# Kernel optimization log

Hardware: AMD Instinct MI355X
Metric: run time of the kernel (lower is better)

The kernel has to match this reference:

```python
import jax, jax.numpy as jnp
import numpy as np

HIDDEN = 4096
NUM_HEADS = 32
NUM_KV_HEADS = 8
HEAD_DIM = 128


def setup_inputs() -> dict:
    key = jax.random.key(0)
    k0, k1, k2, k3, k4 = jax.random.split(key, 5)
    B, S = 1, 2048
    s = 0.02
    return {
        "hidden_states": jax.random.normal(k0, (B, S, HIDDEN), dtype=jnp.float32),
        "Wq": jax.random.normal(k1, (HIDDEN, NUM_HEADS * HEAD_DIM), dtype=jnp.float32) * s,
        "Wk": jax.random.normal(k2, (HIDDEN, NUM_KV_HEADS * HEAD_DIM), dtype=jnp.float32) * s,
        "Wv": jax.random.normal(k3, (HIDDEN, NUM_KV_HEADS * HEAD_DIM), dtype=jnp.float32) * s,
        "Wo": jax.random.normal(k4, (NUM_HEADS * HEAD_DIM, HIDDEN), dtype=jnp.float32) * s,
    }


def reference(hidden_states, Wq, Wk, Wv, Wo):
    B, S, _ = hidden_states.shape
    n_rep = NUM_HEADS // NUM_KV_HEADS
    # Projections -> [B, H, S, D]
    q = (hidden_states @ Wq).reshape(B, S, NUM_HEADS, HEAD_DIM).transpose(0, 2, 1, 3)
    k = (hidden_states @ Wk).reshape(B, S, NUM_KV_HEADS, HEAD_DIM).transpose(0, 2, 1, 3)
    v = (hidden_states @ Wv).reshape(B, S, NUM_KV_HEADS, HEAD_DIM).transpose(0, 2, 1, 3)
    # GQA expansion: repeat_interleave KV heads to match query head count
    k = jnp.repeat(k, n_rep, axis=1)
    v = jnp.repeat(v, n_rep, axis=1)
    scale = HEAD_DIM ** -0.5
    # Full [B, H, S, S] attention scores (faithful to the naive reference)
    scores = jnp.einsum("bhqd,bhkd->bhqk", q, k) * scale
    causal = jnp.tril(jnp.ones((S, S), dtype=bool))
    scores = jnp.where(causal[None, None], scores, jnp.float32(-jnp.inf))
    probs = jax.nn.softmax(scores, axis=-1)
    out = jnp.einsum("bhqk,bhkd->bhqd", probs, v)
    out = out.transpose(0, 2, 1, 3).reshape(B, S, NUM_HEADS * HEAD_DIM)
    return out @ Wo
```

## Files before the change

kernel.cpp:

```cpp
#include <hip/hip_runtime.h>
#include <hip/hip_bf16.h>

typedef __bf16 bf16;
typedef __bf16 bf16x4 __attribute__((ext_vector_type(4)));
typedef __bf16 bf16x8 __attribute__((ext_vector_type(8)));
typedef float  f32x4  __attribute__((ext_vector_type(4)));
typedef float  f32x16 __attribute__((ext_vector_type(16)));
typedef unsigned u32x4 __attribute__((ext_vector_type(4)));

#define SEQ  2048
#define HID  4096
#define QKVN 6144

__device__ __forceinline__ void gload_lds16(const void* g, void* l) {
  __builtin_amdgcn_global_load_lds(
      (const __attribute__((address_space(1))) void*)g,
      (__attribute__((address_space(3))) void*)l, 16, 0, 0);
}

__device__ __forceinline__ unsigned cvtpk(float lo, float hi) {
  unsigned r;
  asm("v_cvt_pk_bf16_f32 %0, %1, %2" : "=v"(r) : "v"(lo), "v"(hi));
  return r;
}
__device__ __forceinline__ void plswap(unsigned& a, unsigned& b) {
  asm("v_permlane32_swap_b32 %0, %1" : "+v"(a), "+v"(b));
}

__global__ __launch_bounds__(256) void cast_f32_bf16(const float* __restrict__ in,
                                                     bf16* __restrict__ out, int n) {
  int i = (blockIdx.x * 256 + threadIdx.x) * 4;
  int stride = gridDim.x * 256 * 4;
  for (; i < n; i += stride) {
    float4 v = *(const float4*)(in + i);
    bf16x4 o;
    o[0] = (bf16)v.x; o[1] = (bf16)v.y; o[2] = (bf16)v.z; o[3] = (bf16)v.w;
    *(bf16x4*)(out + i) = o;
  }
}

__global__ __launch_bounds__(256) void transpose_cast(const float* __restrict__ W,
                                                      bf16* __restrict__ Wt,
                                                      int N, int roff) {
  __shared__ float tile[64][65];
  int k0 = blockIdx.y * 64;
  int n0 = blockIdx.x * 64;
  int t = threadIdx.x;
  int lr = t >> 4;
  int lc = (t & 15) * 4;
#pragma unroll
  for (int p = 0; p < 4; ++p) {
    int row = p * 16 + lr;
    float4 v = *(const float4*)(W + (size_t)(k0 + row) * N + n0 + lc);
    tile[row][lc] = v.x; tile[row][lc + 1] = v.y;
    tile[row][lc + 2] = v.z; tile[row][lc + 3] = v.w;
  }
  __syncthreads();
#pragma unroll
  for (int p = 0; p < 4; ++p) {
    int n = p * 16 + lr;
    bf16x4 o;
#pragma unroll
    for (int q = 0; q < 4; ++q) o[q] = (bf16)tile[lc + q][n];
    *(bf16x4*)(Wt + (size_t)(roff + n0 + n) * 4096 + k0 + lc) = o;
  }
}

__global__ __launch_bounds__(256) void transpose_v(const bf16* __restrict__ QKV,
                                                   bf16* __restrict__ Vt_g) {
  __shared__ bf16 tile[32][33];
  int s0 = blockIdx.x * 32;
  int d0 = blockIdx.y * 32;
  int g  = blockIdx.z;
  int t = threadIdx.x;
  int r = t >> 5, c = t & 31;
#pragma unroll
  for (int p = 0; p < 4; ++p)
    tile[r + p * 8][c] = QKV[(size_t)(s0 + r + p * 8) * QKVN + 5120 + g * 128 + d0 + c];
  __syncthreads();
#pragma unroll
  for (int p = 0; p < 4; ++p)
    Vt_g[(size_t)(g * 128 + d0 + r + p * 8) * SEQ + s0 + c] = tile[c][r + p * 8];
}

template <typename OUT_T>
__global__ __launch_bounds__(256) void gemm_bt(const bf16* __restrict__ A,
                                               const bf16* __restrict__ Bt,
                                               OUT_T* __restrict__ C,
                                               int K, int ldc) {
  __shared__ __align__(16) bf16 Abuf[128 * 64];
  __shared__ __align__(16) bf16 Bbuf[128 * 64];
  int m0 = blockIdx.y * 128, n0 = blockIdx.x * 128;
  int tid = threadIdx.x, w = tid >> 6, lane = tid & 63;
  int wr = w >> 1, wc = w & 1;
  int l15 = lane & 15, l4 = lane >> 4;
  f32x4 acc[4][4] = {};
  const int nk = K >> 6;
  for (int kt = 0; kt < nk; ++kt) {
    int k0 = kt << 6;
#pragma unroll
    for (int p = 0; p < 4; ++p) {
      int c = p * 256 + tid;
      int row = c >> 3, slot = c & 7;
      int ssl = (slot ^ (row & 7)) << 4;
      gload_lds16((const char*)(A + (size_t)(m0 + row) * K + k0) + ssl, (char*)Abuf + c * 16);
      gload_lds16((const char*)(Bt + (size_t)(n0 + row) * K + k0) + ssl, (char*)Bbuf + c * 16);
    }
    __syncthreads();
    bf16x8 af[4][2], bfr[4][2];
#pragma unroll
    for (int m = 0; m < 4; ++m)
#pragma unroll
      for (int kk = 0; kk < 2; ++kk) {
        int row = wr * 64 + m * 16 + l15;
        af[m][kk] = *(const bf16x8*)((const char*)Abuf + row * 128 +
                                     (((kk * 4 + l4) ^ (row & 7)) << 4));
      }
#pragma unroll
    for (int n = 0; n < 4; ++n)
#pragma unroll
      for (int kk = 0; kk < 2; ++kk) {
        int row = wc * 64 + n * 16 + l15;
        bfr[n][kk] = *(const bf16x8*)((const char*)Bbuf + row * 128 +
                                      (((kk * 4 + l4) ^ (row & 7)) << 4));
      }
#pragma unroll
    for (int kk = 0; kk < 2; ++kk)
#pragma unroll
      for (int m = 0; m < 4; ++m)
#pragma unroll
        for (int n = 0; n < 4; ++n)
          acc[m][n] = __builtin_amdgcn_mfma_f32_16x16x32_bf16(af[m][kk], bfr[n][kk],
                                                              acc[m][n], 0, 0, 0);
    __syncthreads();
  }
#pragma unroll
  for (int m = 0; m < 4; ++m)
#pragma unroll
    for (int n = 0; n < 4; ++n)
#pragma unroll
      for (int i = 0; i < 4; ++i) {
        int row = m0 + wr * 64 + m * 16 + l4 * 4 + i;
        int col = n0 + wc * 64 + n * 16 + l15;
        C[(size_t)row * ldc + col] = (OUT_T)acc[m][n][i];
      }
}

__global__ __launch_bounds__(256, 2) void attn_kernel(const bf16* __restrict__ QKV,
                                                      const bf16* __restrict__ Vt_g,
                                                      bf16* __restrict__ attn) {
  __shared__ __align__(16) bf16 Klds[2][64 * 128];
  __shared__ __align__(16) bf16 Vlds[2][64 * 128];
  const int bid = blockIdx.x;
  const int g = bid & 7;
  const int rest = bid >> 3;
  const int hi = rest & 3;
  const int pair = rest >> 2;
  const int qb_a = pair, qb_b = 31 - pair;
  const int tid = threadIdx.x, w = tid >> 6, lane = tid & 63;
  const int l31 = lane & 31, hh = lane >> 5;
  const int head = g * 4 + hi;
  const bool isB = (w < 2);
  const int myqb = isB ? qb_b : qb_a;
  const int unit_q0 = myqb * 64 + (w & 1) * 32;
  const int qcol = head * 128;
  const int kcol = 4096 + g * 128;
  const float scale = 0.08838834764831845f;
  const float LOG2E = 1.4426950408889634f;

  const bf16* Vhead = Vt_g + (size_t)g * 128 * SEQ;

  bf16x8 qf[8];
#pragma unroll
  for (int db = 0; db < 8; ++db)
    qf[db] = *(const bf16x8*)(QKV + (size_t)(unit_q0 + l31) * QKVN + qcol +
                              db * 16 + hh * 8);

  f32x16 acc_o[4] = {};
  float m_run = -1e30f, l_run = 0.f;

  auto stageKV = [&](int kb, int buf) {
#pragma unroll
    for (int j = 0; j < 4; ++j) {
      int c = tid + (j << 8);
      int row = c >> 4, s = c & 15;
      int sl = s ^ (row & 15);
      gload_lds16((const char*)(QKV + (size_t)(kb + row) * QKVN + kcol) + (sl << 4),
                  (char*)Klds[buf] + (c << 4));
      int d = row * 2 + (sl >> 3);
      int ko = (sl & 7) << 3;
      gload_lds16(Vhead + (size_t)d * SEQ + kb + ko, (char*)Vlds[buf] + (c << 4));
    }
  };

  auto compute_unit = [&](int kb, int cur) {
    const char* Kb = (const char*)Klds[cur];
    const char* Vb = (const char*)Vlds[cur];
    f32x16 s0 = {}, s1 = {};
    __builtin_amdgcn_s_setprio(1);
#pragma unroll
    for (int db = 0; db < 8; ++db) {
      int slot = (db * 2 + hh) ^ (l31 & 15);
      bf16x8 k0 = *(const bf16x8*)(Kb + l31 * 256 + slot * 16);
      bf16x8 k1 = *(const bf16x8*)(Kb + (32 + l31) * 256 + slot * 16);
      s0 = __builtin_amdgcn_mfma_f32_32x32x16_bf16(k0, qf[db], s0, 0, 0, 0);
      s1 = __builtin_amdgcn_mfma_f32_32x32x16_bf16(k1, qf[db], s1, 0, 0, 0);
    }
    __builtin_amdgcn_s_setprio(0);
    float p0[16], p1[16];
    const bool needmask = (kb + 64 > unit_q0);
    const int qg = unit_q0 + l31;
#pragma unroll
    for (int r = 0; r < 16; ++r) {
      float v0 = s0[r] * scale, v1 = s1[r] * scale;
      if (needmask) {
        int krow = (r & 3) + 8 * (r >> 2) + 4 * hh;
        if (kb + krow > qg)      v0 = -1e30f;
        if (kb + 32 + krow > qg) v1 = -1e30f;
      }
      p0[r] = v0; p1[r] = v1;
    }
    float t = fmaxf(p0[0], p1[0]);
#pragma unroll
    for (int r = 1; r < 16; ++r) t = fmaxf(t, fmaxf(p0[r], p1[r]));
    t = fmaxf(t, __shfl_xor(t, 32));
    if (!__all(t - m_run <= 8.0f)) {
      float mnew = fmaxf(m_run, t);
      float fac = exp2f((m_run - mnew) * LOG2E);
      m_run = mnew;
      l_run *= fac;
#pragma unroll
      for (int dt = 0; dt < 4; ++dt)
#pragma unroll
        for (int r = 0; r < 16; ++r) acc_o[dt][r] *= fac;
    }
    float psum = 0.f;
#pragma unroll
    for (int r = 0; r < 16; ++r) {
      p0[r] = exp2f((p0[r] - m_run) * LOG2E); psum += p0[r];
      p1[r] = exp2f((p1[r] - m_run) * LOG2E); psum += p1[r];
    }
    psum += __shfl_xor(psum, 32);
    l_run += psum;
    bf16x8 paf[4];
#pragma unroll
    for (int kstep = 0; kstep < 4; ++kstep) {
      const float* p = (kstep < 2) ? p0 : p1;
      const int base = (kstep & 1) * 8;
      unsigned a0 = cvtpk(p[base + 0], p[base + 1]);
      unsigned b0 = cvtpk(p[base + 4], p[base + 5]);
      plswap(a0, b0);
      unsigned a1 = cvtpk(p[base + 2], p[base + 3]);
      unsigned b1 = cvtpk(p[base + 6], p[base + 7]);
      plswap(a1, b1);
      u32x4 pw; pw[0] = a0; pw[1] = a1; pw[2] = b0; pw[3] = b1;
      paf[kstep] = __builtin_bit_cast(bf16x8, pw);
    }
    __builtin_amdgcn_s_setprio(1);
#pragma unroll
    for (int dt = 0; dt < 4; ++dt) {
      int vrow = dt * 16 + (l31 >> 1);
#pragma unroll
      for (int kstep = 0; kstep < 4; ++kstep) {
        int slot = ((l31 & 1) * 8 + kstep * 2 + hh) ^ (vrow & 15);
        bf16x8 vf = *(const bf16x8*)(Vb + vrow * 256 + slot * 16);
        acc_o[dt] = __builtin_amdgcn_mfma_f32_32x32x16_bf16(vf, paf[kstep], acc_o[dt], 0, 0, 0);
      }
    }
    __builtin_amdgcn_s_setprio(0);
  };

  stageKV(0, 0);
  __syncthreads();

  int cur = 0;
  for (int kbi = 0; kbi <= qb_b; ++kbi) {
    int kb = kbi * 64;
    if (kbi < qb_b) stageKV(kb + 64, cur ^ 1);
    if (isB || kbi <= qb_a) compute_unit(kb, cur);
    __syncthreads();
    cur ^= 1;
  }

  float inv_l = 1.0f / l_run;
  bf16* orow = attn + (size_t)(unit_q0 + l31) * 4096 + qcol;
#pragma unroll
  for (int dt = 0; dt < 4; ++dt)
#pragma unroll
    for (int r = 0; r < 16; ++r) {
      int d = dt * 32 + (r & 3) + 8 * (r >> 2) + 4 * hh;
      orow[d] = (bf16)(acc_o[dt][r] * inv_l);
    }
}

extern "C" void kernel_launch(void* const* d_in, const int* in_sizes, int n_in,
                              void* d_out, int out_size, void* d_ws, size_t ws_size,
                              hipStream_t stream) {
  const float* X  = (const float*)d_in[0];
  const float* Wq = (const float*)d_in[1];
  const float* Wk = (const float*)d_in[2];
  const float* Wv = (const float*)d_in[3];
  const float* Wo = (const float*)d_in[4];
  float* out = (float*)d_out;

  const size_t XB_OFF  = 0;
  const size_t WT_OFF  = 16777216;
  const size_t VT_OFF  = WT_OFF + 33554432;
  const size_t QKV_OFF = 16777216 + 50331648;
  if (ws_size < (size_t)92274688) return;

  char* ws = (char*)d_ws;
  bf16* Xb    = (bf16*)(ws + XB_OFF);
  bf16* Wt    = (bf16*)(ws + WT_OFF);
  bf16* Vt_g  = (bf16*)(ws + VT_OFF);
  bf16* QKV   = (bf16*)(ws + QKV_OFF);
  bf16* attnb = Xb;

  cast_f32_bf16<<<2048, 256, 0, stream>>>(X, Xb, SEQ * HID);
  transpose_cast<<<dim3(4096 / 64, 4096 / 64), 256, 0, stream>>>(Wq, Wt, 4096, 0);
  transpose_cast<<<dim3(1024 / 64, 4096 / 64), 256, 0, stream>>>(Wk, Wt, 1024, 4096);
  transpose_cast<<<dim3(1024 / 64, 4096 / 64), 256, 0, stream>>>(Wv, Wt, 1024, 5120);
  gemm_bt<bf16><<<dim3(QKVN / 128, SEQ / 128), 256, 0, stream>>>(Xb, Wt, QKV, HID, QKVN);
  transpose_cast<<<dim3(4096 / 64, 4096 / 64), 256, 0, stream>>>(Wo, Wt, 4096, 0);
  transpose_v<<<dim3(SEQ / 32, 4, 8), 256, 0, stream>>>(QKV, Vt_g);
  attn_kernel<<<512, 256, 0, stream>>>(QKV, Vt_g, attnb);
  gemm_bt<float><<<dim3(4096 / 128, SEQ / 128), 256, 0, stream>>>(attnb, Wt, out, HID, 4096);
}
```

Before: 369.8 us.

## Fuse weight transpose and bf16 cast into GEMM B-tile loads

Drops the separate transpose_cast kernels for Wq/Wk/Wv/Wo. The GEMMs now read the fp32 weights directly in their natural K-major layout, convert them to bf16 in registers, store them to LDS, and fetch MFMA B fragments with ds_read_b64_tr_b16 transposed LDS reads. This removes a full read/write pass over 64 MB of fp32 weights and the bf16 Wt workspace. In exchange each GEMM block reads fp32 weights (twice the bytes) on every tile, once per M-block, through synchronous register loads instead of async global_load_lds.

```diff
diff --git a/kernel.cpp b/kernel.cpp
--- a/kernel.cpp
+++ b/kernel.cpp
@@ -7,6 +7,7 @@
 typedef float  f32x4  __attribute__((ext_vector_type(4)));
 typedef float  f32x16 __attribute__((ext_vector_type(16)));
 typedef unsigned u32x4 __attribute__((ext_vector_type(4)));
+typedef __attribute__((address_space(3))) char lds_char;
 
 #define SEQ  2048
 #define HID  4096
@@ -39,33 +40,6 @@
   }
 }
 
-__global__ __launch_bounds__(256) void transpose_cast(const float* __restrict__ W,
-                                                      bf16* __restrict__ Wt,
-                                                      int N, int roff) {
-  __shared__ float tile[64][65];
-  int k0 = blockIdx.y * 64;
-  int n0 = blockIdx.x * 64;
-  int t = threadIdx.x;
-  int lr = t >> 4;
-  int lc = (t & 15) * 4;
-#pragma unroll
-  for (int p = 0; p < 4; ++p) {
-    int row = p * 16 + lr;
-    float4 v = *(const float4*)(W + (size_t)(k0 + row) * N + n0 + lc);
-    tile[row][lc] = v.x; tile[row][lc + 1] = v.y;
-    tile[row][lc + 2] = v.z; tile[row][lc + 3] = v.w;
-  }
-  __syncthreads();
-#pragma unroll
-  for (int p = 0; p < 4; ++p) {
-    int n = p * 16 + lr;
-    bf16x4 o;
-#pragma unroll
-    for (int q = 0; q < 4; ++q) o[q] = (bf16)tile[lc + q][n];
-    *(bf16x4*)(Wt + (size_t)(roff + n0 + n) * 4096 + k0 + lc) = o;
-  }
-}
-
 __global__ __launch_bounds__(256) void transpose_v(const bf16* __restrict__ QKV,
                                                    bf16* __restrict__ Vt_g) {
   __shared__ bf16 tile[32][33];
@@ -84,30 +58,57 @@
 }
 
 template <typename OUT_T>
-__global__ __launch_bounds__(256) void gemm_bt(const bf16* __restrict__ A,
-                                               const bf16* __restrict__ Bt,
-                                               OUT_T* __restrict__ C,
-                                               int K, int ldc) {
+__global__ __launch_bounds__(256) void gemm_trb(const bf16* __restrict__ A,
+                                                const float* __restrict__ W0,
+                                                const float* __restrict__ W1,
+                                                const float* __restrict__ W2,
+                                                OUT_T* __restrict__ C,
+                                                int K, int ldc) {
   __shared__ __align__(16) bf16 Abuf[128 * 64];
-  __shared__ __align__(16) bf16 Bbuf[128 * 64];
+  __shared__ __align__(16) bf16 Bbuf[64 * 128];
   int m0 = blockIdx.y * 128, n0 = blockIdx.x * 128;
+  const float* W; int Wn, n0l;
+  if (n0 < 4096)      { W = W0; Wn = 4096; n0l = n0; }
+  else if (n0 < 5120) { W = W1; Wn = 1024; n0l = n0 - 4096; }
+  else                { W = W2; Wn = 1024; n0l = n0 - 5120; }
   int tid = threadIdx.x, w = tid >> 6, lane = tid & 63;
   int wr = w >> 1, wc = w & 1;
   int l15 = lane & 15, l4 = lane >> 4;
   f32x4 acc[4][4] = {};
+  lds_char* const bbase = (lds_char*)(char*)Bbuf + wc * 512 + l4 * 2048 + l15 * 8;
   const int nk = K >> 6;
   for (int kt = 0; kt < nk; ++kt) {
     int k0 = kt << 6;
+    float4 bv0[4], bv1[4];
+#pragma unroll
+    for (int p = 0; p < 4; ++p) {
+      int c = p * 256 + tid;
+      int kq = c >> 4, n8 = (c & 15) * 8;
+      const float* src = W + (size_t)(k0 + kq) * Wn + n0l + n8;
+      bv0[p] = *(const float4*)src;
+      bv1[p] = *(const float4*)(src + 4);
+    }
 #pragma unroll
     for (int p = 0; p < 4; ++p) {
       int c = p * 256 + tid;
       int row = c >> 3, slot = c & 7;
       int ssl = (slot ^ (row & 7)) << 4;
       gload_lds16((const char*)(A + (size_t)(m0 + row) * K + k0) + ssl, (char*)Abuf + c * 16);
-      gload_lds16((const char*)(Bt + (size_t)(n0 + row) * K + k0) + ssl, (char*)Bbuf + c * 16);
+    }
+#pragma unroll
+    for (int p = 0; p < 4; ++p) {
+      int c = p * 256 + tid;
+      int kq = c >> 4, n8 = (c & 15) * 8;
+      u32x4 pw;
+      pw[0] = cvtpk(bv0[p].x, bv0[p].y);
+      pw[1] = cvtpk(bv0[p].z, bv0[p].w);
+      pw[2] = cvtpk(bv1[p].x, bv1[p].y);
+      pw[3] = cvtpk(bv1[p].z, bv1[p].w);
+      int boff = (kq >> 2) * 1024 + (n8 >> 4) * 128 + (kq & 3) * 32 + (n8 & 15) * 2;
+      *(u32x4*)((char*)Bbuf + boff) = pw;
     }
     __syncthreads();
-    bf16x8 af[4][2], bfr[4][2];
+    bf16x8 af[4][2];
 #pragma unroll
     for (int m = 0; m < 4; ++m)
 #pragma unroll
@@ -116,13 +117,29 @@
         af[m][kk] = *(const bf16x8*)((const char*)Abuf + row * 128 +
                                      (((kk * 4 + l4) ^ (row & 7)) << 4));
       }
-#pragma unroll
-    for (int n = 0; n < 4; ++n)
+    unsigned long long tr[4][2][2];
+#pragma unroll
+    for (int nf = 0; nf < 4; ++nf)
+#pragma unroll
+      for (int kk = 0; kk < 2; ++kk)
+#pragma unroll
+        for (int h = 0; h < 2; ++h)
+          asm volatile("ds_read_b64_tr_b16 %0, %1 offset:%c2"
+                       : "=v"(tr[nf][kk][h])
+                       : "v"(bbase), "i"(kk * 8192 + h * 1024 + nf * 128));
+    asm volatile("s_waitcnt lgkmcnt(0)" ::: "memory");
+    __builtin_amdgcn_sched_barrier(0);
+    bf16x8 bfr[4][2];
+#pragma unroll
+    for (int nf = 0; nf < 4; ++nf)
 #pragma unroll
       for (int kk = 0; kk < 2; ++kk) {
-        int row = wc * 64 + n * 16 + l15;
-        bfr[n][kk] = *(const bf16x8*)((const char*)Bbuf + row * 128 +
-                                      (((kk * 4 + l4) ^ (row & 7)) << 4));
+        u32x4 pw;
+        pw[0] = (unsigned)(tr[nf][kk][0]);
+        pw[1] = (unsigned)(tr[nf][kk][0] >> 32);
+        pw[2] = (unsigned)(tr[nf][kk][1]);
+        pw[3] = (unsigned)(tr[nf][kk][1] >> 32);
+        bfr[nf][kk] = __builtin_bit_cast(bf16x8, pw);
       }
 #pragma unroll
     for (int kk = 0; kk < 2; ++kk)
@@ -304,25 +321,21 @@
   float* out = (float*)d_out;
 
   const size_t XB_OFF  = 0;
-  const size_t WT_OFF  = 16777216;
-  const size_t VT_OFF  = WT_OFF + 33554432;
-  const size_t QKV_OFF = 16777216 + 50331648;
-  if (ws_size < (size_t)92274688) return;
+  const size_t VT_OFF  = 16777216;
+  const size_t QKV_OFF = 16777216 + 4194304;
+  if (ws_size < (size_t)(QKV_OFF + 25165824)) return;
 
   char* ws = (char*)d_ws;
   bf16* Xb    = (bf16*)(ws + XB_OFF);
-  bf16* Wt    = (bf16*)(ws + WT_OFF);
   bf16* Vt_g  = (bf16*)(ws + VT_OFF);
   bf16* QKV   = (bf16*)(ws + QKV_OFF);
   bf16* attnb = Xb;
 
   cast_f32_bf16<<<2048, 256, 0, stream>>>(X, Xb, SEQ * HID);
-  transpose_cast<<<dim3(4096 / 64, 4096 / 64), 256, 0, stream>>>(Wq, Wt, 4096, 0);
-  transpose_cast<<<dim3(1024 / 64, 4096 / 64), 256, 0, stream>>>(Wk, Wt, 1024, 4096);
-  transpose_cast<<<dim3(1024 / 64, 4096 / 64), 256, 0, stream>>>(Wv, Wt, 1024, 5120);
-  gemm_bt<bf16><<<dim3(QKVN / 128, SEQ / 128), 256, 0, stream>>>(Xb, Wt, QKV, HID, QKVN);
-  transpose_cast<<<dim3(4096 / 64, 4096 / 64), 256, 0, stream>>>(Wo, Wt, 4096, 0);
+  gemm_trb<bf16><<<dim3(QKVN / 128, SEQ / 128), 256, 0, stream>>>(
+      Xb, Wq, Wk, Wv, QKV, HID, QKVN);
   transpose_v<<<dim3(SEQ / 32, 4, 8), 256, 0, stream>>>(QKV, Vt_g);
   attn_kernel<<<512, 256, 0, stream>>>(QKV, Vt_g, attnb);
-  gemm_bt<float><<<dim3(4096 / 128, SEQ / 128), 256, 0, stream>>>(attnb, Wt, out, HID, 4096);
-}
+  gemm_trb<float><<<dim3(4096 / 128, SEQ / 128), 256, 0, stream>>>(
+      attnb, Wo, Wo, Wo, out, HID, 4096);
+}
```

Result: slower. 377.4 us (+2.0%).

## Load V fragments directly from global into registers, drop V LDS staging

Applied to the files above, without the earlier changes.

Removes the double-buffered V tile from shared memory and has each lane load its transposed-V MFMA operand fragments straight from global memory (L2), prefetching the next d-tile while the current one's MFMAs run. Halving LDS use allows raising launch bounds to three blocks per CU for more occupancy. The trade-off is redundant global/L2 traffic, since every wave re-reads V rather than sharing it through LDS, along with exposed global-load latency inside the PV loop and tighter register budgets.

```diff
diff --git a/kernel.cpp b/kernel.cpp
--- a/kernel.cpp
+++ b/kernel.cpp
@@ -146,11 +146,10 @@
       }
 }
 
-__global__ __launch_bounds__(256, 2) void attn_kernel(const bf16* __restrict__ QKV,
+__global__ __launch_bounds__(256, 3) void attn_kernel(const bf16* __restrict__ QKV,
                                                       const bf16* __restrict__ Vt_g,
                                                       bf16* __restrict__ attn) {
   __shared__ __align__(16) bf16 Klds[2][64 * 128];
-  __shared__ __align__(16) bf16 Vlds[2][64 * 128];
   const int bid = blockIdx.x;
   const int g = bid & 7;
   const int rest = bid >> 3;
@@ -169,6 +168,7 @@
   const float LOG2E = 1.4426950408889634f;
 
   const bf16* Vhead = Vt_g + (size_t)g * 128 * SEQ;
+  const bf16* vlane = Vhead + (size_t)l31 * SEQ + hh * 8;
 
   bf16x8 qf[8];
 #pragma unroll
@@ -179,7 +179,7 @@
   f32x16 acc_o[4] = {};
   float m_run = -1e30f, l_run = 0.f;
 
-  auto stageKV = [&](int kb, int buf) {
+  auto stageK = [&](int kb, int buf) {
 #pragma unroll
     for (int j = 0; j < 4; ++j) {
       int c = tid + (j << 8);
@@ -187,15 +187,11 @@
       int sl = s ^ (row & 15);
       gload_lds16((const char*)(QKV + (size_t)(kb + row) * QKVN + kcol) + (sl << 4),
                   (char*)Klds[buf] + (c << 4));
-      int d = row * 2 + (sl >> 3);
-      int ko = (sl & 7) << 3;
-      gload_lds16(Vhead + (size_t)d * SEQ + kb + ko, (char*)Vlds[buf] + (c << 4));
     }
   };
 
   auto compute_unit = [&](int kb, int cur) {
     const char* Kb = (const char*)Klds[cur];
-    const char* Vb = (const char*)Vlds[cur];
     f32x16 s0 = {}, s1 = {};
     __builtin_amdgcn_s_setprio(1);
 #pragma unroll
@@ -207,6 +203,11 @@
       s1 = __builtin_amdgcn_mfma_f32_32x32x16_bf16(k1, qf[db], s1, 0, 0, 0);
     }
     __builtin_amdgcn_s_setprio(0);
+    const bf16* vb0 = vlane + kb;
+    bf16x8 vc[4];
+#pragma unroll
+    for (int ks = 0; ks < 4; ++ks)
+      vc[ks] = *(const bf16x8*)(vb0 + ks * 16);
     float p0[16], p1[16];
     const bool needmask = (kb + 64 > unit_q0);
     const int qg = unit_q0 + l31;
@@ -259,24 +260,29 @@
     __builtin_amdgcn_s_setprio(1);
 #pragma unroll
     for (int dt = 0; dt < 4; ++dt) {
-      int vrow = dt * 16 + (l31 >> 1);
-#pragma unroll
-      for (int kstep = 0; kstep < 4; ++kstep) {
-        int slot = ((l31 & 1) * 8 + kstep * 2 + hh) ^ (vrow & 15);
-        bf16x8 vf = *(const bf16x8*)(Vb + vrow * 256 + slot * 16);
-        acc_o[dt] = __builtin_amdgcn_mfma_f32_32x32x16_bf16(vf, paf[kstep], acc_o[dt], 0, 0, 0);
-      }
+      bf16x8 vn[4];
+      if (dt < 3) {
+        const bf16* nb = vb0 + (size_t)(dt + 1) * 32 * SEQ;
+#pragma unroll
+        for (int ks = 0; ks < 4; ++ks)
+          vn[ks] = *(const bf16x8*)(nb + ks * 16);
+      }
+#pragma unroll
+      for (int ks = 0; ks < 4; ++ks)
+        acc_o[dt] = __builtin_amdgcn_mfma_f32_32x32x16_bf16(vc[ks], paf[ks], acc_o[dt], 0, 0, 0);
+#pragma unroll
+      for (int ks = 0; ks < 4; ++ks) vc[ks] = vn[ks];
     }
     __builtin_amdgcn_s_setprio(0);
   };
 
-  stageKV(0, 0);
+  stageK(0, 0);
   __syncthreads();
 
   int cur = 0;
   for (int kbi = 0; kbi <= qb_b; ++kbi) {
     int kb = kbi * 64;
-    if (kbi < qb_b) stageKV(kb + 64, cur ^ 1);
+    if (kbi < qb_b) stageK(kb + 64, cur ^ 1);
     if (isB || kbi <= qb_a) compute_unit(kb, cur);
     __syncthreads();
     cur ^= 1;
```

Result: slower. 522.7 us (+41.3%).
